# Kernel optimization log

Hardware: AMD Instinct MI355X
Metric: run time of the kernel (lower is better)

The kernel has to match this reference:

```python
import jax, jax.numpy as jnp
import numpy as np
import math

B, S, D_MODEL, H = 2, 2048, 1024, 16
D_HEAD = D_MODEL // H
THETA = 10000.0


def _init_linear(key, out_f, in_f):
    std = math.sqrt(2.0 / (out_f + in_f))
    w = jax.random.truncated_normal(key, -3.0, 3.0, (out_f, in_f), dtype=jnp.float32)
    return w * std


def setup_inputs() -> dict:
    key = jax.random.key(0)
    k1, k2, k3 = jax.random.split(key, 3)
    x = jax.random.normal(k1, (B, S, D_MODEL), dtype=jnp.float32)
    wqkv = _init_linear(k2, 3 * D_MODEL, D_MODEL)
    w_out = _init_linear(k3, D_MODEL, D_MODEL)
    # RoPE tables: positions [max_seq_len,1] * inv_freq [d_head//2]
    positions = jnp.arange(S, dtype=jnp.float32)[:, None]
    freqs = jnp.arange(0, D_HEAD, 2, dtype=jnp.float32) / D_HEAD
    inv_freq = 1.0 / (THETA ** freqs)
    angles = positions * inv_freq  # [S, D_HEAD//2]
    cos = jnp.cos(angles)
    sin = jnp.sin(angles)
    token_positions = jnp.arange(S, dtype=jnp.int32)
    return {"x": x, "wqkv": wqkv, "w_out": w_out, "cos": cos, "sin": sin,
            "token_positions": token_positions}


def _apply_rope(t, cos_pos, sin_pos):
    # t: [b, h, s, d], cos/sin_pos: [s, d//2] broadcast over b,h
    te = t[..., 0::2]
    to = t[..., 1::2]
    re = te * cos_pos - to * sin_pos
    ro = te * sin_pos + to * cos_pos
    # interleave even/odd back: [..., d//2, 2] -> [..., d]
    out = jnp.stack([re, ro], axis=-1)
    return out.reshape(t.shape)


def reference(x, wqkv, w_out, cos, sin, token_positions):
    b, s, d_model = x.shape
    qkv = jnp.einsum('oi,bsi->bso', wqkv, x)  # [b, s, 3*d_model]
    q, k, v = jnp.split(qkv, 3, axis=-1)

    def to_heads(t):
        return t.reshape(b, s, H, D_HEAD).transpose(0, 2, 1, 3)  # b h s d

    q, k, v = to_heads(q), to_heads(k), to_heads(v)

    cos_pos = cos[token_positions]  # [s, d_head//2]
    sin_pos = sin[token_positions]
    q = _apply_rope(q, cos_pos, sin_pos)
    k = _apply_rope(k, cos_pos, sin_pos)

    scores = jnp.einsum('bhqd,bhkd->bhqk', q, k) / math.sqrt(D_HEAD)
    causal = jnp.tril(jnp.ones((s, s), dtype=bool))  # ~triu(diag=1)
    scores = jnp.where(causal, scores, -jnp.inf)
    weights = jax.nn.softmax(scores, axis=-1)
    y = jnp.einsum('bhqk,bhkd->bhqd', weights, v)
    y = y.transpose(0, 2, 1, 3).reshape(b, s, d_model)
    return jnp.einsum('oi,bsi->bso', w_out, y)
```

## Files before the change

kernel.cpp:

```cpp
#include <hip/hip_runtime.h>
#include <hip/hip_bf16.h>


#define S_LEN 2048
#define DMODEL 1024
#define NH 16
#define QKVN 3072

typedef __attribute__((ext_vector_type(4))) short short4v;
typedef __attribute__((ext_vector_type(8))) short short8v;
typedef __attribute__((ext_vector_type(4))) float floatx4;

#define CSOFT 0.18033688f

__device__ __forceinline__ unsigned short f2bf(float f) {
  unsigned int u = __float_as_uint(f);
  u += 0x7FFFu + ((u >> 16) & 1u);
  return (unsigned short)(u >> 16);
}
__device__ __forceinline__ float bf2f(unsigned short u) {
  return __uint_as_float(((unsigned int)u) << 16);
}
__device__ __forceinline__ void gload16(const void* g, void* l) {
  __builtin_amdgcn_global_load_lds((const __attribute__((address_space(1))) void*)g,
                                   (__attribute__((address_space(3))) void*)l,
                                   16, 0, 0);
}
__device__ __forceinline__ int perm4(int c) {
  return (c >> 3) * 32 + (c & 3) * 8 + ((c >> 2) & 1) * 4;
}

__global__ __launch_bounds__(256) void cast_bf16_perm_k(const float* __restrict__ in,
                                                        unsigned short* __restrict__ out,
                                                        int nchunk) {
  int i = blockIdx.x * 256 + threadIdx.x;
  if (i >= nchunk) return;
  int c = i & 3;
  const float4* f4 = reinterpret_cast<const float4*>(in);
  float4 lo = f4[(i >> 2) * 8 + c];
  float4 hi = f4[(i >> 2) * 8 + 4 + c];
  short8v o;
  o[0] = (short)f2bf(lo.x); o[1] = (short)f2bf(lo.y);
  o[2] = (short)f2bf(lo.z); o[3] = (short)f2bf(lo.w);
  o[4] = (short)f2bf(hi.x); o[5] = (short)f2bf(hi.y);
  o[6] = (short)f2bf(hi.z); o[7] = (short)f2bf(hi.w);
  reinterpret_cast<short8v*>(out)[i] = o;
}

template <bool OUT_BF16>
__global__ __launch_bounds__(256) void gemm_bt(const unsigned short* __restrict__ A,
                                               const unsigned short* __restrict__ Bm,
                                               void* __restrict__ Cp, int M, int N, int K) {
  __shared__ __align__(16) unsigned short As[2][128 * 32];
  __shared__ __align__(16) unsigned short Bs[2][128 * 32];
  const int tid = threadIdx.x;
  const int lane = tid & 63;
  const int w = tid >> 6;
  const int wm = w >> 1, wn = w & 1;
  const int l15 = lane & 15, l4 = lane >> 4;
  const int bm = blockIdx.y * 128, bn = blockIdx.x * 128;
  const int srow = lane >> 2;
  const int schunk = ((lane & 3) - ((lane >> 3) & 3)) & 3;
  const int rslot = (l4 + (l15 >> 1)) & 3;

  floatx4 acc[4][4] = {};
  const int nt = K >> 5;

#define GSTAGE(T, BUF)                                                                   \
  {                                                                                      \
    const int k0s = (T) << 5;                                                            \
    _Pragma("unroll") for (int j = 0; j < 2; ++j) {                                      \
      const unsigned short* ga =                                                         \
          A + (size_t)(bm + j * 64 + w * 16 + srow) * K + k0s + schunk * 8;              \
      gload16(ga, &As[BUF][j * 2048 + w * 512]);                                         \
      const unsigned short* gb =                                                         \
          Bm + (size_t)(bn + j * 64 + w * 16 + srow) * K + k0s + schunk * 8;             \
      gload16(gb, &Bs[BUF][j * 2048 + w * 512]);                                         \
    }                                                                                    \
  }

#define GBODY(T, BUF)                                                                    \
  {                                                                                      \
    if ((T) + 1 < nt) {                                                                  \
      GSTAGE((T) + 1, BUF ^ 1);                                                          \
      asm volatile("s_waitcnt vmcnt(4)" ::: "memory");                                   \
    } else {                                                                             \
      asm volatile("s_waitcnt vmcnt(0)" ::: "memory");                                   \
    }                                                                                    \
    __syncthreads();                                                                     \
    short8v af[4], bfr[4];                                                               \
    _Pragma("unroll") for (int f = 0; f < 4; ++f) {                                      \
      af[f]  = *(const short8v*)(&As[BUF][(wm * 64 + f * 16 + l15) * 32 + rslot * 8]);   \
      bfr[f] = *(const short8v*)(&Bs[BUF][(wn * 64 + f * 16 + l15) * 32 + rslot * 8]);   \
    }                                                                                    \
    _Pragma("unroll") for (int f = 0; f < 4; ++f)                                        \
      _Pragma("unroll") for (int g = 0; g < 4; ++g)                                      \
        acc[f][g] = __builtin_amdgcn_mfma_f32_16x16x32_bf16(af[f], bfr[g], acc[f][g], 0, 0, 0); \
    __syncthreads();                                                                     \
  }

  GSTAGE(0, 0);
  for (int t = 0; t < nt; t += 2) {
    GBODY(t, 0);
    GBODY(t + 1, 1);
  }
#undef GBODY
#undef GSTAGE

#pragma unroll
  for (int f = 0; f < 4; ++f)
#pragma unroll
    for (int g = 0; g < 4; ++g)
#pragma unroll
      for (int r = 0; r < 4; ++r) {
        int row = bm + wm * 64 + f * 16 + l4 * 4 + r;
        int col = bn + wn * 64 + g * 16 + l15;
        if (OUT_BF16)
          ((unsigned short*)Cp)[(size_t)row * N + col] = f2bf(acc[f][g][r]);
        else
          ((float*)Cp)[(size_t)row * N + col] = acc[f][g][r];
      }
}

__global__ __launch_bounds__(256) void rope_pack_k(const unsigned short* __restrict__ qkvb,
                                                   unsigned short* __restrict__ qp_,
                                                   unsigned short* __restrict__ kp_,
                                                   unsigned short* __restrict__ vtp_,
                                                   const float* __restrict__ cosp,
                                                   const float* __restrict__ sinp,
                                                   const int* __restrict__ tpos) {
  __shared__ unsigned short Vs[64][68];
  const int tid = threadIdx.x;
  const int bh = blockIdx.x >> 5;
  const int st = blockIdx.x & 31;
  const int b = bh >> 4, h = bh & 15;
  const int c = tid & 15, t0 = tid >> 4;
  const int s0 = st * 64;
  const int pc = perm4(c);

#pragma unroll
  for (int it = 0; it < 4; ++it) {
    const int tl = it * 16 + t0;
    const int s = s0 + tl;
    const int tp = tpos[s];
    const size_t base = ((size_t)(b * S_LEN + s)) * QKVN + h * 64 + c * 4;
    const float co0 = cosp[tp * 32 + 2 * c], si0 = sinp[tp * 32 + 2 * c];
    const float co1 = cosp[tp * 32 + 2 * c + 1], si1 = sinp[tp * 32 + 2 * c + 1];
    {
      const float c0 = co0 * CSOFT, s0q = si0 * CSOFT;
      const float c1 = co1 * CSOFT, s1q = si1 * CSOFT;
      ushort4 rv = *(const ushort4*)(qkvb + base);
      float a0 = bf2f(rv.x), a1 = bf2f(rv.y), a2 = bf2f(rv.z), a3 = bf2f(rv.w);
      ushort4 ov;
      ov.x = f2bf(a0 * c0 - a1 * s0q); ov.y = f2bf(a0 * s0q + a1 * c0);
      ov.z = f2bf(a2 * c1 - a3 * s1q); ov.w = f2bf(a2 * s1q + a3 * c1);
      *(ushort4*)(qp_ + ((size_t)bh * S_LEN + s) * 64 + pc) = ov;
    }
    {
      ushort4 rv = *(const ushort4*)(qkvb + base + DMODEL);
      float a0 = bf2f(rv.x), a1 = bf2f(rv.y), a2 = bf2f(rv.z), a3 = bf2f(rv.w);
      ushort4 ov;
      ov.x = f2bf(a0 * co0 - a1 * si0); ov.y = f2bf(a0 * si0 + a1 * co0);
      ov.z = f2bf(a2 * co1 - a3 * si1); ov.w = f2bf(a2 * si1 + a3 * co1);
      *(ushort4*)(kp_ + ((size_t)bh * S_LEN + s) * 64 + pc) = ov;
    }
    {
      ushort4 rv = *(const ushort4*)(qkvb + base + 2 * DMODEL);
      *(ushort4*)(&Vs[tl][c * 4]) = rv;
    }
  }
  __syncthreads();
#pragma unroll
  for (int it = 0; it < 4; ++it) {
    const int d = it * 16 + t0;
    ushort4 ov;
    ov.x = Vs[c * 4 + 0][d]; ov.y = Vs[c * 4 + 1][d];
    ov.z = Vs[c * 4 + 2][d]; ov.w = Vs[c * 4 + 3][d];
    *(ushort4*)(vtp_ + ((size_t)bh * 64 + d) * S_LEN + s0 + pc) = ov;
  }
}

__device__ __forceinline__ short8v readfrag128(const unsigned short* L, int row, int cc) {
  return *(const short8v*)(L + row * 64 + (((cc) ^ (row & 7)) << 3));
}

__device__ __forceinline__ void stage_tiles(const unsigned short* kg0, const unsigned short* vg0,
                                            int kt, unsigned short* Kb, unsigned short* Vb,
                                            int tid, int w) {
#pragma unroll
  for (int i = 0; i < 2; ++i) {
    int jj = i * 256 + tid;
    int row = jj >> 3;
    int cc = (jj & 7) ^ (row & 7);
    gload16(kg0 + (size_t)kt * 4096 + row * 64 + cc * 8, Kb + (i * 256 + w * 64) * 8);
    gload16(vg0 + (size_t)row * S_LEN + kt * 64 + cc * 8, Vb + (i * 256 + w * 64) * 8);
  }
}

__global__ __launch_bounds__(256) void attn_mfma(const unsigned short* __restrict__ qp_,
                                                 const unsigned short* __restrict__ kp_,
                                                 const unsigned short* __restrict__ vtp_,
                                                 unsigned short* __restrict__ yb) {
  __shared__ __align__(16) unsigned short Kl[2][4096];
  __shared__ __align__(16) unsigned short Vl[2][4096];
  const int tid = threadIdx.x;
  const int lane = tid & 63, w = tid >> 6;
  const int l15 = lane & 15, l4 = lane >> 4;
  const int j = blockIdx.x;
  const int bh = (j & 7) + 8 * ((j >> 3) & 3);
  const int qt = 31 - (j >> 5);
  const int b = bh >> 4, h = bh & 15;

  const unsigned short* kg0 = kp_ + (size_t)bh * S_LEN * 64;
  const unsigned short* vg0 = vtp_ + (size_t)bh * 64 * S_LEN;

  const unsigned short* qp = qp_ + ((size_t)bh * S_LEN + qt * 64 + w * 16 + l15) * 64;
  short8v qf[2];
#pragma unroll
  for (int c2 = 0; c2 < 2; ++c2)
    qf[c2] = *(const short8v*)(qp + c2 * 32 + l4 * 8);

  floatx4 o[4] = {};
  float mrun = -1e30f, lsum = 0.f;

  stage_tiles(kg0, vg0, 0, Kl[0], Vl[0], tid, w);

  for (int kt = 0; kt <= qt; ++kt) {
    const int cur = kt & 1;
    if (kt < qt) {
      stage_tiles(kg0, vg0, kt + 1, Kl[cur ^ 1], Vl[cur ^ 1], tid, w);
      asm volatile("s_waitcnt vmcnt(4)" ::: "memory");
    } else {
      asm volatile("s_waitcnt vmcnt(0)" ::: "memory");
    }
    __syncthreads();

    const unsigned short* Kc = Kl[cur];
    const unsigned short* Vc = Vl[cur];
    const bool diag = (kt == qt);
    float s_[4][4];
    __builtin_amdgcn_s_setprio(1);
#pragma unroll
    for (int g = 0; g < 4; ++g) {
      if (diag && g > w) {
        s_[g][0] = s_[g][1] = s_[g][2] = s_[g][3] = -INFINITY;
        continue;
      }
      short8v k0 = readfrag128(Kc, g * 16 + l15, l4);
      short8v k1 = readfrag128(Kc, g * 16 + l15, 4 + l4);
      floatx4 t = {0.f, 0.f, 0.f, 0.f};
      t = __builtin_amdgcn_mfma_f32_16x16x32_bf16(k0, qf[0], t, 0, 0, 0);
      t = __builtin_amdgcn_mfma_f32_16x16x32_bf16(k1, qf[1], t, 0, 0, 0);
#pragma unroll
      for (int r = 0; r < 4; ++r) {
        float v = t[r];
        if (diag && g == w && (l4 * 4 + r > l15)) v = -INFINITY;
        s_[g][r] = v;
      }
    }
    __builtin_amdgcn_s_setprio(0);

    float tm = -INFINITY;
#pragma unroll
    for (int g = 0; g < 4; ++g)
#pragma unroll
      for (int r = 0; r < 4; ++r) tm = fmaxf(tm, s_[g][r]);
    tm = fmaxf(tm, __shfl_xor(tm, 16));
    tm = fmaxf(tm, __shfl_xor(tm, 32));

    if (!__all(tm <= mrun + 3.0f)) {
      float nm = fmaxf(mrun, tm);
      float rs = exp2f(mrun - nm);
      mrun = nm;
      lsum *= rs;
      float rsr[4];
#pragma unroll
      for (int r = 0; r < 4; ++r) rsr[r] = __shfl(rs, l4 * 4 + r);
#pragma unroll
      for (int dt = 0; dt < 4; ++dt)
#pragma unroll
        for (int r = 0; r < 4; ++r) o[dt][r] *= rsr[r];
    }

    union { unsigned short u[16]; short8v v[2]; } pk;
    float psum = 0.f;
#pragma unroll
    for (int g = 0; g < 4; ++g)
#pragma unroll
      for (int r = 0; r < 4; ++r) {
        float p = exp2f(s_[g][r] - mrun);
        psum += p;
        pk.u[g * 4 + r] = (unsigned short)(__float_as_uint(p) >> 16);
      }
    lsum += psum;

    __builtin_amdgcn_s_setprio(1);
#pragma unroll
    for (int dt = 0; dt < 4; ++dt) {
      short8v v0 = readfrag128(Vc, dt * 16 + l15, l4);
      short8v v1 = readfrag128(Vc, dt * 16 + l15, 4 + l4);
      o[dt] = __builtin_amdgcn_mfma_f32_16x16x32_bf16(pk.v[0], v0, o[dt], 0, 0, 0);
      o[dt] = __builtin_amdgcn_mfma_f32_16x16x32_bf16(pk.v[1], v1, o[dt], 0, 0, 0);
    }
    __builtin_amdgcn_s_setprio(0);
    __syncthreads();
  }

  lsum += __shfl_xor(lsum, 16);
  lsum += __shfl_xor(lsum, 32);
  float linv = 1.f / lsum;
  float lr[4];
#pragma unroll
  for (int r = 0; r < 4; ++r) lr[r] = __shfl(linv, l4 * 4 + r);
#pragma unroll
  for (int dt = 0; dt < 4; ++dt)
#pragma unroll
    for (int r = 0; r < 4; ++r) {
      size_t row = (size_t)(b * S_LEN + qt * 64 + w * 16 + l4 * 4 + r);
      int col = (h * 2 + (dt >> 1)) * 32 + (l15 >> 2) * 8 + (l15 & 3) + 4 * (dt & 1);
      yb[row * DMODEL + col] = f2bf(o[dt][r] * lr[r]);
    }
}

extern "C" void kernel_launch(void* const* d_in, const int* in_sizes, int n_in,
                              void* d_out, int out_size, void* d_ws, size_t ws_size,
                              hipStream_t stream) {
  const float* x     = (const float*)d_in[0];
  const float* wqkv  = (const float*)d_in[1];
  const float* w_out = (const float*)d_in[2];
  const float* cosp  = (const float*)d_in[3];
  const float* sinp  = (const float*)d_in[4];
  const int*   tpos  = (const int*)d_in[5];
  float* out = (float*)d_out;
  char* ws = (char*)d_ws;

  const size_t MB = 1024 * 1024;
  unsigned short* xb    = (unsigned short*)(ws + 0);
  unsigned short* wqkvb = (unsigned short*)(ws + 8 * MB);
  unsigned short* wob   = (unsigned short*)(ws + 14 * MB);
  unsigned short* qkvb  = (unsigned short*)(ws + 16 * MB);
  unsigned short* qpk   = (unsigned short*)(ws + 40 * MB);
  unsigned short* kpk   = (unsigned short*)(ws + 48 * MB);
  unsigned short* vtpk  = (unsigned short*)(ws + 56 * MB);
  unsigned short* yb    = (unsigned short*)(ws + 0);

  cast_bf16_perm_k<<<2048, 256, 0, stream>>>(x, xb, 524288);
  cast_bf16_perm_k<<<1536, 256, 0, stream>>>(wqkv, wqkvb, 393216);
  cast_bf16_perm_k<<<512, 256, 0, stream>>>(w_out, wob, 131072);

  gemm_bt<true><<<dim3(24, 32), 256, 0, stream>>>(xb, wqkvb, qkvb, 4096, QKVN, 1024);

  rope_pack_k<<<1024, 256, 0, stream>>>(qkvb, qpk, kpk, vtpk, cosp, sinp, tpos);

  attn_mfma<<<1024, 256, 0, stream>>>(qpk, kpk, vtpk, yb);

  gemm_bt<false><<<dim3(8, 32), 256, 0, stream>>>(yb, wob, out, 4096, DMODEL, 1024);
}
```

Before: 201.3 us.

## Pair causal query tiles per attention block and fuse the three cast kernels

Each attention block now processes two query tiles, qt=31-p and qt=p, against the same streamed K/V tiles. This balances causal work across blocks, halves the grid, and reuses each staged K/V tile for both query tiles. The three fp32→bf16 cast launches are merged into one kernel that picks its source and destination by index range, saving two launches. The cost is more registers for the doubled accumulators, fewer blocks in flight, and more serialized work per block.

```diff
diff --git a/kernel.cpp b/kernel.cpp
--- a/kernel.cpp
+++ b/kernel.cpp
@@ -30,21 +30,29 @@
   return (c >> 3) * 32 + (c & 3) * 8 + ((c >> 2) & 1) * 4;
 }
 
-__global__ __launch_bounds__(256) void cast_bf16_perm_k(const float* __restrict__ in,
-                                                        unsigned short* __restrict__ out,
-                                                        int nchunk) {
+__global__ __launch_bounds__(256) void cast_all_k(const float* __restrict__ x,
+                                                  const float* __restrict__ wqkv,
+                                                  const float* __restrict__ wout,
+                                                  unsigned short* __restrict__ xb,
+                                                  unsigned short* __restrict__ wqkvb,
+                                                  unsigned short* __restrict__ wob) {
   int i = blockIdx.x * 256 + threadIdx.x;
-  if (i >= nchunk) return;
-  int c = i & 3;
+  const float* in;
+  unsigned short* out;
+  int base;
+  if (i < 524288)       { in = x;    out = xb;    base = i; }
+  else if (i < 917504)  { in = wqkv; out = wqkvb; base = i - 524288; }
+  else                  { in = wout; out = wob;   base = i - 917504; }
+  int c = base & 3;
   const float4* f4 = reinterpret_cast<const float4*>(in);
-  float4 lo = f4[(i >> 2) * 8 + c];
-  float4 hi = f4[(i >> 2) * 8 + 4 + c];
+  float4 lo = f4[(base >> 2) * 8 + c];
+  float4 hi = f4[(base >> 2) * 8 + 4 + c];
   short8v o;
   o[0] = (short)f2bf(lo.x); o[1] = (short)f2bf(lo.y);
   o[2] = (short)f2bf(lo.z); o[3] = (short)f2bf(lo.w);
   o[4] = (short)f2bf(hi.x); o[5] = (short)f2bf(hi.y);
   o[6] = (short)f2bf(hi.z); o[7] = (short)f2bf(hi.w);
-  reinterpret_cast<short8v*>(out)[i] = o;
+  reinterpret_cast<short8v*>(out)[base] = o;
 }
 
 template <bool OUT_BF16>
@@ -208,26 +216,31 @@
   const int l15 = lane & 15, l4 = lane >> 4;
   const int j = blockIdx.x;
   const int bh = (j & 7) + 8 * ((j >> 3) & 3);
-  const int qt = 31 - (j >> 5);
+  const int p = j >> 5;
+  const int qtA = 31 - p;
+  const int qtB = p;
   const int b = bh >> 4, h = bh & 15;
 
   const unsigned short* kg0 = kp_ + (size_t)bh * S_LEN * 64;
   const unsigned short* vg0 = vtp_ + (size_t)bh * 64 * S_LEN;
 
-  const unsigned short* qp = qp_ + ((size_t)bh * S_LEN + qt * 64 + w * 16 + l15) * 64;
-  short8v qf[2];
-#pragma unroll
-  for (int c2 = 0; c2 < 2; ++c2)
-    qf[c2] = *(const short8v*)(qp + c2 * 32 + l4 * 8);
-
-  floatx4 o[4] = {};
-  float mrun = -1e30f, lsum = 0.f;
+  const unsigned short* qpA = qp_ + ((size_t)bh * S_LEN + qtA * 64 + w * 16 + l15) * 64;
+  const unsigned short* qpB = qp_ + ((size_t)bh * S_LEN + qtB * 64 + w * 16 + l15) * 64;
+  short8v qfA[2], qfB[2];
+#pragma unroll
+  for (int c2 = 0; c2 < 2; ++c2) {
+    qfA[c2] = *(const short8v*)(qpA + c2 * 32 + l4 * 8);
+    qfB[c2] = *(const short8v*)(qpB + c2 * 32 + l4 * 8);
+  }
+
+  floatx4 oA[4] = {}, oB[4] = {};
+  float mA = -1e30f, lA = 0.f, mB = -1e30f, lB = 0.f;
 
   stage_tiles(kg0, vg0, 0, Kl[0], Vl[0], tid, w);
 
-  for (int kt = 0; kt <= qt; ++kt) {
+  for (int kt = 0; kt <= qtA; ++kt) {
     const int cur = kt & 1;
-    if (kt < qt) {
+    if (kt < qtA) {
       stage_tiles(kg0, vg0, kt + 1, Kl[cur ^ 1], Vl[cur ^ 1], tid, w);
       asm volatile("s_waitcnt vmcnt(4)" ::: "memory");
     } else {
@@ -237,89 +250,153 @@
 
     const unsigned short* Kc = Kl[cur];
     const unsigned short* Vc = Vl[cur];
-    const bool diag = (kt == qt);
-    float s_[4][4];
+    const bool actB = (kt <= qtB);
+
+    float sA[4][4], sB[4][4];
     __builtin_amdgcn_s_setprio(1);
 #pragma unroll
     for (int g = 0; g < 4; ++g) {
-      if (diag && g > w) {
-        s_[g][0] = s_[g][1] = s_[g][2] = s_[g][3] = -INFINITY;
+      const bool diagA = (kt == qtA);
+      if (diagA && g > w) {
+        sA[g][0] = sA[g][1] = sA[g][2] = sA[g][3] = -INFINITY;
+        if (actB) { sB[g][0] = sB[g][1] = sB[g][2] = sB[g][3] = -INFINITY; }
         continue;
       }
       short8v k0 = readfrag128(Kc, g * 16 + l15, l4);
       short8v k1 = readfrag128(Kc, g * 16 + l15, 4 + l4);
-      floatx4 t = {0.f, 0.f, 0.f, 0.f};
-      t = __builtin_amdgcn_mfma_f32_16x16x32_bf16(k0, qf[0], t, 0, 0, 0);
-      t = __builtin_amdgcn_mfma_f32_16x16x32_bf16(k1, qf[1], t, 0, 0, 0);
+      floatx4 tA = {0.f, 0.f, 0.f, 0.f};
+      tA = __builtin_amdgcn_mfma_f32_16x16x32_bf16(k0, qfA[0], tA, 0, 0, 0);
+      tA = __builtin_amdgcn_mfma_f32_16x16x32_bf16(k1, qfA[1], tA, 0, 0, 0);
 #pragma unroll
       for (int r = 0; r < 4; ++r) {
-        float v = t[r];
-        if (diag && g == w && (l4 * 4 + r > l15)) v = -INFINITY;
-        s_[g][r] = v;
+        float v = tA[r];
+        if (diagA && g == w && (l4 * 4 + r > l15)) v = -INFINITY;
+        sA[g][r] = v;
+      }
+      if (actB) {
+        const bool diagB = (kt == qtB);
+        if (diagB && g > w) {
+          sB[g][0] = sB[g][1] = sB[g][2] = sB[g][3] = -INFINITY;
+        } else {
+          floatx4 tB = {0.f, 0.f, 0.f, 0.f};
+          tB = __builtin_amdgcn_mfma_f32_16x16x32_bf16(k0, qfB[0], tB, 0, 0, 0);
+          tB = __builtin_amdgcn_mfma_f32_16x16x32_bf16(k1, qfB[1], tB, 0, 0, 0);
+#pragma unroll
+          for (int r = 0; r < 4; ++r) {
+            float v = tB[r];
+            if (diagB && g == w && (l4 * 4 + r > l15)) v = -INFINITY;
+            sB[g][r] = v;
+          }
+        }
       }
     }
     __builtin_amdgcn_s_setprio(0);
 
-    float tm = -INFINITY;
-#pragma unroll
-    for (int g = 0; g < 4; ++g)
-#pragma unroll
-      for (int r = 0; r < 4; ++r) tm = fmaxf(tm, s_[g][r]);
-    tm = fmaxf(tm, __shfl_xor(tm, 16));
-    tm = fmaxf(tm, __shfl_xor(tm, 32));
-
-    if (!__all(tm <= mrun + 3.0f)) {
-      float nm = fmaxf(mrun, tm);
-      float rs = exp2f(mrun - nm);
-      mrun = nm;
-      lsum *= rs;
-      float rsr[4];
-#pragma unroll
-      for (int r = 0; r < 4; ++r) rsr[r] = __shfl(rs, l4 * 4 + r);
-#pragma unroll
-      for (int dt = 0; dt < 4; ++dt)
-#pragma unroll
-        for (int r = 0; r < 4; ++r) o[dt][r] *= rsr[r];
-    }
-
-    union { unsigned short u[16]; short8v v[2]; } pk;
-    float psum = 0.f;
-#pragma unroll
-    for (int g = 0; g < 4; ++g)
-#pragma unroll
-      for (int r = 0; r < 4; ++r) {
-        float p = exp2f(s_[g][r] - mrun);
-        psum += p;
-        pk.u[g * 4 + r] = (unsigned short)(__float_as_uint(p) >> 16);
-      }
-    lsum += psum;
-
+    union { unsigned short u[16]; short8v v[2]; } pkA, pkB;
+    {
+      float tm = -INFINITY;
+#pragma unroll
+      for (int g = 0; g < 4; ++g)
+#pragma unroll
+        for (int r = 0; r < 4; ++r) tm = fmaxf(tm, sA[g][r]);
+      tm = fmaxf(tm, __shfl_xor(tm, 16));
+      tm = fmaxf(tm, __shfl_xor(tm, 32));
+      if (!__all(tm <= mA + 3.0f)) {
+        float nm = fmaxf(mA, tm);
+        float rs = exp2f(mA - nm);
+        mA = nm;
+        lA *= rs;
+        float rsr[4];
+#pragma unroll
+        for (int r = 0; r < 4; ++r) rsr[r] = __shfl(rs, l4 * 4 + r);
+#pragma unroll
+        for (int dt = 0; dt < 4; ++dt)
+#pragma unroll
+          for (int r = 0; r < 4; ++r) oA[dt][r] *= rsr[r];
+      }
+      float psum = 0.f;
+#pragma unroll
+      for (int g = 0; g < 4; ++g)
+#pragma unroll
+        for (int r = 0; r < 4; ++r) {
+          float pv = exp2f(sA[g][r] - mA);
+          psum += pv;
+          pkA.u[g * 4 + r] = (unsigned short)(__float_as_uint(pv) >> 16);
+        }
+      lA += psum;
+    }
     __builtin_amdgcn_s_setprio(1);
 #pragma unroll
     for (int dt = 0; dt < 4; ++dt) {
       short8v v0 = readfrag128(Vc, dt * 16 + l15, l4);
       short8v v1 = readfrag128(Vc, dt * 16 + l15, 4 + l4);
-      o[dt] = __builtin_amdgcn_mfma_f32_16x16x32_bf16(pk.v[0], v0, o[dt], 0, 0, 0);
-      o[dt] = __builtin_amdgcn_mfma_f32_16x16x32_bf16(pk.v[1], v1, o[dt], 0, 0, 0);
+      oA[dt] = __builtin_amdgcn_mfma_f32_16x16x32_bf16(pkA.v[0], v0, oA[dt], 0, 0, 0);
+      oA[dt] = __builtin_amdgcn_mfma_f32_16x16x32_bf16(pkA.v[1], v1, oA[dt], 0, 0, 0);
     }
     __builtin_amdgcn_s_setprio(0);
+
+    if (actB) {
+      float tm = -INFINITY;
+#pragma unroll
+      for (int g = 0; g < 4; ++g)
+#pragma unroll
+        for (int r = 0; r < 4; ++r) tm = fmaxf(tm, sB[g][r]);
+      tm = fmaxf(tm, __shfl_xor(tm, 16));
+      tm = fmaxf(tm, __shfl_xor(tm, 32));
+      if (!__all(tm <= mB + 3.0f)) {
+        float nm = fmaxf(mB, tm);
+        float rs = exp2f(mB - nm);
+        mB = nm;
+        lB *= rs;
+        float rsr[4];
+#pragma unroll
+        for (int r = 0; r < 4; ++r) rsr[r] = __shfl(rs, l4 * 4 + r);
+#pragma unroll
+        for (int dt = 0; dt < 4; ++dt)
+#pragma unroll
+          for (int r = 0; r < 4; ++r) oB[dt][r] *= rsr[r];
+      }
+      float psum = 0.f;
+#pragma unroll
+      for (int g = 0; g < 4; ++g)
+#pragma unroll
+        for (int r = 0; r < 4; ++r) {
+          float pv = exp2f(sB[g][r] - mB);
+          psum += pv;
+          pkB.u[g * 4 + r] = (unsigned short)(__float_as_uint(pv) >> 16);
+        }
+      lB += psum;
+      __builtin_amdgcn_s_setprio(1);
+#pragma unroll
+      for (int dt = 0; dt < 4; ++dt) {
+        short8v v0 = readfrag128(Vc, dt * 16 + l15, l4);
+        short8v v1 = readfrag128(Vc, dt * 16 + l15, 4 + l4);
+        oB[dt] = __builtin_amdgcn_mfma_f32_16x16x32_bf16(pkB.v[0], v0, oB[dt], 0, 0, 0);
+        oB[dt] = __builtin_amdgcn_mfma_f32_16x16x32_bf16(pkB.v[1], v1, oB[dt], 0, 0, 0);
+      }
+      __builtin_amdgcn_s_setprio(0);
+    }
     __syncthreads();
   }
 
-  lsum += __shfl_xor(lsum, 16);
-  lsum += __shfl_xor(lsum, 32);
-  float linv = 1.f / lsum;
-  float lr[4];
-#pragma unroll
-  for (int r = 0; r < 4; ++r) lr[r] = __shfl(linv, l4 * 4 + r);
-#pragma unroll
-  for (int dt = 0; dt < 4; ++dt)
-#pragma unroll
-    for (int r = 0; r < 4; ++r) {
-      size_t row = (size_t)(b * S_LEN + qt * 64 + w * 16 + l4 * 4 + r);
-      int col = (h * 2 + (dt >> 1)) * 32 + (l15 >> 2) * 8 + (l15 & 3) + 4 * (dt & 1);
-      yb[row * DMODEL + col] = f2bf(o[dt][r] * lr[r]);
-    }
+#define EPILOGUE(QT, OV, LV)                                                           \
+  {                                                                                    \
+    float ls = (LV);                                                                   \
+    ls += __shfl_xor(ls, 16);                                                          \
+    ls += __shfl_xor(ls, 32);                                                          \
+    float linv = 1.f / ls;                                                             \
+    float lr[4];                                                                       \
+    _Pragma("unroll") for (int r = 0; r < 4; ++r) lr[r] = __shfl(linv, l4 * 4 + r);    \
+    _Pragma("unroll") for (int dt = 0; dt < 4; ++dt)                                   \
+      _Pragma("unroll") for (int r = 0; r < 4; ++r) {                                  \
+        size_t row = (size_t)(b * S_LEN + (QT) * 64 + w * 16 + l4 * 4 + r);            \
+        int col = (h * 2 + (dt >> 1)) * 32 + (l15 >> 2) * 8 + (l15 & 3) + 4 * (dt & 1);\
+        yb[row * DMODEL + col] = f2bf((OV)[dt][r] * lr[r]);                            \
+      }                                                                                \
+  }
+  EPILOGUE(qtA, oA, lA);
+  EPILOGUE(qtB, oB, lB);
+#undef EPILOGUE
 }
 
 extern "C" void kernel_launch(void* const* d_in, const int* in_sizes, int n_in,
@@ -344,15 +421,13 @@
   unsigned short* vtpk  = (unsigned short*)(ws + 56 * MB);
   unsigned short* yb    = (unsigned short*)(ws + 0);
 
-  cast_bf16_perm_k<<<2048, 256, 0, stream>>>(x, xb, 524288);
-  cast_bf16_perm_k<<<1536, 256, 0, stream>>>(wqkv, wqkvb, 393216);
-  cast_bf16_perm_k<<<512, 256, 0, stream>>>(w_out, wob, 131072);
+  cast_all_k<<<4096, 256, 0, stream>>>(x, wqkv, w_out, xb, wqkvb, wob);
 
   gemm_bt<true><<<dim3(24, 32), 256, 0, stream>>>(xb, wqkvb, qkvb, 4096, QKVN, 1024);
 
   rope_pack_k<<<1024, 256, 0, stream>>>(qkvb, qpk, kpk, vtpk, cosp, sinp, tpos);
 
-  attn_mfma<<<1024, 256, 0, stream>>>(qpk, kpk, vtpk, yb);
+  attn_mfma<<<512, 256, 0, stream>>>(qpk, kpk, vtpk, yb);
 
   gemm_bt<false><<<dim3(8, 32), 256, 0, stream>>>(yb, wob, out, 4096, DMODEL, 1024);
 }
```

After: 199.2 us. Within noise of the previous version (-1.0%).
